# Kernel optimization log

Hardware: AMD Instinct MI355X
Metric: run time of the kernel (lower is better)

## Reference

```python
import jax, jax.numpy as jnp
import numpy as np

B, N, C = 8, 4096, 256
HEADS = 8
DH = C // HEADS
SR = 4
EPS = 1e-5


def setup_inputs() -> dict:
    key = jax.random.key(0)
    ks = jax.random.split(key, 12)
    s = 0.02
    inp = {
        "x": jax.random.normal(ks[0], (B, N, C), dtype=jnp.float32),
        "H": 64,
        "W": 64,
        # nn.Linear weights stored torch-style [out, in]
        "q_w": jax.random.normal(ks[1], (C, C), dtype=jnp.float32) * s,
        "q_b": jax.random.normal(ks[2], (C,), dtype=jnp.float32) * s,
        "kv_w": jax.random.normal(ks[3], (2 * C, C), dtype=jnp.float32) * s,
        "kv_b": jax.random.normal(ks[4], (2 * C,), dtype=jnp.float32) * s,
        # Conv2d weight torch OIHW [C, C, SR, SR]
        "sr_w": jax.random.normal(ks[5], (C, C, SR, SR), dtype=jnp.float32) * s,
        "sr_b": jax.random.normal(ks[6], (C,), dtype=jnp.float32) * s,
        "ln_g": jnp.ones((C,), dtype=jnp.float32),
        "ln_b": jnp.zeros((C,), dtype=jnp.float32),
        "proj_w": jax.random.normal(ks[7], (C, C), dtype=jnp.float32) * s,
        "proj_b": jax.random.normal(ks[8], (C,), dtype=jnp.float32) * s,
    }
    return inp


def _layernorm(x, g, b):
    mu = jnp.mean(x, axis=-1, keepdims=True)
    var = jnp.mean(jnp.square(x - mu), axis=-1, keepdims=True)
    return (x - mu) * jax.lax.rsqrt(var + EPS) * g + b


def reference(x, H, W, q_w, q_b, kv_w, kv_b, sr_w, sr_b, ln_g, ln_b, proj_w, proj_b):
    b, n, c = x.shape
    scale = 1.0 / jnp.sqrt(jnp.float32(DH))

    # q projection -> [b, heads, n, dh]
    q = (x @ q_w.T + q_b).reshape(b, n, HEADS, DH).transpose(0, 2, 1, 3)

    # spatial reduction: conv stride=SR kernel=SR on the [b,H,W,c] image
    x_img = x.reshape(b, H, W, c)  # NHWC
    kern = jnp.transpose(sr_w, (2, 3, 1, 0))  # OIHW -> HWIO
    x_sr = jax.lax.conv_general_dilated(
        x_img, kern, window_strides=(SR, SR), padding="VALID",
        dimension_numbers=("NHWC", "HWIO", "NHWC")) + sr_b
    n_kv = (H // SR) * (W // SR)
    x_sr = x_sr.reshape(b, n_kv, c)
    x_sr = _layernorm(x_sr, ln_g, ln_b)

    # kv projection -> k, v: [b, heads, n_kv, dh]
    kv = (x_sr @ kv_w.T + kv_b).reshape(b, n_kv, 2, HEADS, DH)
    kv = kv.transpose(2, 0, 3, 1, 4)
    k, v = kv[0], kv[1]

    # attention (dropout rates are 0.0 / eval mode)
    attn = jnp.einsum("bhnd,bhmd->bhnm", q, k) * scale
    attn = jax.nn.softmax(attn, axis=-1)
    out = jnp.einsum("bhnm,bhmd->bhnd", attn, v)
    out = out.transpose(0, 2, 1, 3).reshape(b, n, c)
    return out @ proj_w.T + proj_b
```

## Files before the change

### kernel.cpp

```cpp
#include <hip/hip_runtime.h>

typedef unsigned short u16;
typedef float f32x4 __attribute__((ext_vector_type(4)));
typedef __bf16 bf16x4 __attribute__((ext_vector_type(4)));
typedef __bf16 bf16x8 __attribute__((ext_vector_type(8)));

#define B_ 8
#define N_ 4096
#define C_ 256
#define NKV 256
#define CEXP 0.25506604f

__device__ inline u16 f2bf(float f) {
    union { float f; unsigned u; } v; v.f = f;
    unsigned r = v.u + 0x7FFF + ((v.u >> 16) & 1);
    return (u16)(r >> 16);
}

__device__ inline void gload16(const void* g, void* l) {
    __builtin_amdgcn_global_load_lds(
        (const __attribute__((address_space(1))) void*)g,
        (__attribute__((address_space(3))) void*)l, 16, 0, 0);
}

__global__ __launch_bounds__(256) void prep_all(
    const float* __restrict__ x, u16* __restrict__ xb,
    const float* __restrict__ qw, const float* __restrict__ kvw,
    const float* __restrict__ pw, const float* __restrict__ srw,
    u16* __restrict__ wqb, u16* __restrict__ wkv, u16* __restrict__ wp, u16* __restrict__ wsr)
{
    size_t base = ((size_t)blockIdx.x * 256 + threadIdx.x) * 4;
    float4 v = *(const float4*)(x + base);
    ushort4 o;
    o.x = f2bf(v.x); o.y = f2bf(v.y); o.z = f2bf(v.z); o.w = f2bf(v.w);
    *(ushort4*)(xb + base) = o;

    int t = blockIdx.x * 256 + threadIdx.x;
    int stride = gridDim.x * 256;
    for (int i = t; i < 65536; i += stride) { wqb[i] = f2bf(qw[i]); wp[i] = f2bf(pw[i]); }
    for (int i = t; i < 131072; i += stride) wkv[i] = f2bf(kvw[i]);
    for (int i = t; i < 1048576; i += stride) {
        int oo = i >> 12, kk = i & 4095;
        int ci = kk & 255, khkw = kk >> 8;
        wsr[i] = f2bf(srw[(size_t)(oo * 256 + ci) * 16 + khkw]);
    }
}

template<int OUTMODE, bool IM2COL>
__device__ __forceinline__ void gemm_body(
    u16* As, u16* Bs,
    const u16* __restrict__ A, const u16* __restrict__ Bt,
    const float* __restrict__ bias, void* __restrict__ outp,
    int M, int Nn, int K, int kchunk, int bm, int bn, int bz)
{
    const int tid = threadIdx.x;
    const int k0 = bz * kchunk;
    const int wid = tid >> 6, lane = tid & 63;
    const int wr = wid >> 1, wc = wid & 1;
    const int lrow = lane & 15, lkg = lane >> 4;

    f32x4 acc[4][4] = {};

    const int c1 = tid, c2 = tid + 256;
    const int r1 = c1 >> 2, cl1 = (c1 & 3) * 8;
    const int r2 = c2 >> 2, cl2 = (c2 & 3) * 8;
    const u16 *aS1, *aS2;
    if constexpr (IM2COL) {
        const int g1 = bm * 128 + r1, g2 = bm * 128 + r2;
        const int b1 = g1 >> 8, p1 = g1 & 255;
        const int b2 = g2 >> 8, p2 = g2 & 255;
        aS1 = A + ((size_t)(b1 * 4096 + (p1 >> 4) * 256 + (p1 & 15) * 4) * 256 + cl1);
        aS2 = A + ((size_t)(b2 * 4096 + (p2 >> 4) * 256 + (p2 & 15) * 4) * 256 + cl2);
    } else {
        aS1 = A + (size_t)(bm * 128 + r1) * K + k0 + cl1;
        aS2 = A + (size_t)(bm * 128 + r2) * K + k0 + cl2;
    }
    const u16* bS1 = Bt + (size_t)(bn * 128 + r1) * K + k0 + cl1;
    const u16* bS2 = Bt + (size_t)(bn * 128 + r2) * K + k0 + cl2;
    u16* aD1 = As + c1 * 8;  u16* aD2 = As + c2 * 8;
    u16* bD1 = Bs + c1 * 8;  u16* bD2 = Bs + c2 * 8;

    for (int kk = 0; kk < kchunk; kk += 32) {
        int aoff;
        if constexpr (IM2COL) {
            const int K0 = k0 + kk;
            const int khkw = K0 >> 8;
            aoff = ((khkw >> 2) * 64 + (khkw & 3)) * 256 + (K0 & 255);
        } else {
            aoff = kk;
        }
        gload16(aS1 + aoff, aD1);
        gload16(aS2 + aoff, aD2);
        gload16(bS1 + kk, bD1);
        gload16(bS2 + kk, bD2);
        __syncthreads();
        bf16x8 af[4], bff[4];
#pragma unroll
        for (int i = 0; i < 4; ++i) {
            af[i]  = *(const bf16x8*)(As + (wr * 64 + i * 16 + lrow) * 32 + lkg * 8);
            bff[i] = *(const bf16x8*)(Bs + (wc * 64 + i * 16 + lrow) * 32 + lkg * 8);
        }
#pragma unroll
        for (int i = 0; i < 4; ++i)
#pragma unroll
            for (int j = 0; j < 4; ++j)
                acc[i][j] = __builtin_amdgcn_mfma_f32_16x16x32_bf16(af[i], bff[j], acc[i][j], 0, 0, 0);
        __syncthreads();
    }

    const int row0 = bm * 128 + wr * 64;
    const int col0 = bn * 128 + wc * 64;
    if constexpr (OUTMODE == 2) {
        float* o = (float*)outp + (size_t)bz * M * Nn;
#pragma unroll
        for (int i = 0; i < 4; ++i)
#pragma unroll
            for (int j = 0; j < 4; ++j)
#pragma unroll
                for (int reg = 0; reg < 4; ++reg)
                    o[(size_t)(row0 + i * 16 + lkg * 4 + reg) * Nn + col0 + j * 16 + lrow] = acc[i][j][reg];
    } else {
#pragma unroll
        for (int j = 0; j < 4; ++j) {
            const int col = col0 + j * 16 + lrow;
            float bv = bias[col];
#pragma unroll
            for (int i = 0; i < 4; ++i)
#pragma unroll
                for (int reg = 0; reg < 4; ++reg) {
                    const size_t idx = (size_t)(row0 + i * 16 + lkg * 4 + reg) * Nn + col;
                    const float val = acc[i][j][reg] + bv;
                    if constexpr (OUTMODE == 1) ((u16*)outp)[idx] = f2bf(val);
                    else                        ((float*)outp)[idx] = val;
                }
        }
    }
}

template<int OUTMODE, bool IM2COL>
__global__ __launch_bounds__(256, 2) void gemm128(
    const u16* __restrict__ A, const u16* __restrict__ Bt,
    const float* __restrict__ bias, void* __restrict__ outp,
    int M, int Nn, int K, int kchunk)
{
    __shared__ __align__(16) u16 As[128 * 32];
    __shared__ __align__(16) u16 Bs[128 * 32];
    gemm_body<OUTMODE, IM2COL>(As, Bs, A, Bt, bias, outp, M, Nn, K, kchunk,
                               blockIdx.x, blockIdx.y, blockIdx.z);
}

__global__ __launch_bounds__(256, 2) void fused_convq(
    const u16* __restrict__ xb, const u16* __restrict__ wsr, float* __restrict__ part,
    const u16* __restrict__ wqb, const float* __restrict__ qb, u16* __restrict__ qbuf)
{
    __shared__ __align__(16) u16 As[128 * 32];
    __shared__ __align__(16) u16 Bs[128 * 32];
    const int id = blockIdx.x;
    if (id < 128) {
        const int z = id & 3, t = id >> 2;
        gemm_body<2, true>(As, Bs, xb, wsr, nullptr, part,
                           2048, 256, 4096, 1024, t >> 1, t & 1, z);
    } else {
        const int qid = id - 128;
        gemm_body<1, false>(As, Bs, xb, wqb, qb, qbuf,
                            32768, 256, 256, 256, qid >> 1, qid & 1, 0);
    }
}

__global__ __launch_bounds__(256) void ln_kernel(
    const float* __restrict__ part, const float* __restrict__ srb,
    const float* __restrict__ g, const float* __restrict__ bb, u16* __restrict__ out)
{
    const int row = blockIdx.x, c = threadIdx.x;
    const size_t idx = (size_t)row * 256 + c;
    float v = srb[c];
#pragma unroll
    for (int z = 0; z < 4; ++z) v += part[idx + (size_t)z * 524288];
    float s = v;
#pragma unroll
    for (int m = 1; m < 64; m <<= 1) s += __shfl_xor(s, m);
    __shared__ float red[4];
    if ((c & 63) == 0) red[c >> 6] = s;
    __syncthreads();
    float tot = red[0] + red[1] + red[2] + red[3];
    float mu = tot * (1.0f / 256.0f);
    float d = v - mu;
    float s2 = d * d;
#pragma unroll
    for (int m = 1; m < 64; m <<= 1) s2 += __shfl_xor(s2, m);
    __syncthreads();
    if ((c & 63) == 0) red[c >> 6] = s2;
    __syncthreads();
    float var = (red[0] + red[1] + red[2] + red[3]) * (1.0f / 256.0f);
    out[idx] = f2bf(d * rsqrtf(var + 1e-5f) * g[c] + bb[c]);
}

__global__ __launch_bounds__(256, 2) void gemm64_kv(
    const u16* __restrict__ A, const u16* __restrict__ Bt,
    const float* __restrict__ bias, u16* __restrict__ outp)
{
    __shared__ __align__(16) u16 As[64 * 32];
    __shared__ __align__(16) u16 Bs[64 * 32];
    const int tid = threadIdx.x, bm = blockIdx.x, bn = blockIdx.y;
    const int wid = tid >> 6, lane = tid & 63;
    const int wr = wid >> 1, wc = wid & 1;
    const int lrow = lane & 15, lkg = lane >> 4;

    f32x4 acc[2][2] = {};
    const int r = tid >> 2, cl = (tid & 3) * 8;
    const u16* aS = A  + (size_t)(bm * 64 + r) * 256 + cl;
    const u16* bS = Bt + (size_t)(bn * 64 + r) * 256 + cl;
    u16* aD = As + tid * 8;
    u16* bD = Bs + tid * 8;

    for (int kk = 0; kk < 256; kk += 32) {
        gload16(aS + kk, aD);
        gload16(bS + kk, bD);
        __syncthreads();
        bf16x8 af[2], bf2[2];
#pragma unroll
        for (int i = 0; i < 2; ++i) {
            af[i]  = *(const bf16x8*)(As + (wr * 32 + i * 16 + lrow) * 32 + lkg * 8);
            bf2[i] = *(const bf16x8*)(Bs + (wc * 32 + i * 16 + lrow) * 32 + lkg * 8);
        }
#pragma unroll
        for (int i = 0; i < 2; ++i)
#pragma unroll
            for (int j = 0; j < 2; ++j)
                acc[i][j] = __builtin_amdgcn_mfma_f32_16x16x32_bf16(af[i], bf2[j], acc[i][j], 0, 0, 0);
        __syncthreads();
    }

    const int row0 = bm * 64 + wr * 32;
    const int col0 = bn * 64 + wc * 32;
#pragma unroll
    for (int j = 0; j < 2; ++j) {
        const int col = col0 + j * 16 + lrow;
        const float bv = bias[col];
        const float sc = (col < 256) ? CEXP : 1.0f;
#pragma unroll
        for (int i = 0; i < 2; ++i)
#pragma unroll
            for (int reg = 0; reg < 4; ++reg)
                outp[(size_t)(row0 + i * 16 + lkg * 4 + reg) * 512 + col] =
                    f2bf((acc[i][j][reg] + bv) * sc);
    }
}

__global__ __launch_bounds__(256, 4) void attn_kernel(
    const u16* __restrict__ qbuf, const u16* __restrict__ kvbuf, u16* __restrict__ obuf)
{
    __shared__ __align__(16) u16 Ks[256 * 32];
    __shared__ __align__(16) u16 Vt[32 * 264];
    const int qt = blockIdx.x, h = blockIdx.y, b = blockIdx.z;
    const int tid = threadIdx.x;
    const int wid = tid >> 6, lane = tid & 63;
    const int lrow = lane & 15, lkg = lane >> 4;

    {
        const int loff = (lane * 16) ^ (((lane >> 3) & 7) << 4);
        const int rloc = loff >> 6, piece = (loff >> 4) & 3;
#pragma unroll
        for (int i = 0; i < 4; ++i) {
            const int c = wid * 4 + i;
            const u16* src = kvbuf + (size_t)(b * 256 + c * 16 + rloc) * 512 + h * 32 + piece * 8;
            gload16(src, Ks + c * 512);
        }
    }
    {
        const int i = tid & 127, dbase = (tid >> 7) * 16;
        const u16* vs0 = kvbuf + (size_t)(b * 256 + 2 * i) * 512 + 256 + h * 32 + dbase;
        const u16* vs1 = vs0 + 512;
        ushort4 a0 = *(const ushort4*)(vs0);
        ushort4 a1 = *(const ushort4*)(vs0 + 4);
        ushort4 a2 = *(const ushort4*)(vs0 + 8);
        ushort4 a3 = *(const ushort4*)(vs0 + 12);
        ushort4 b0 = *(const ushort4*)(vs1);
        ushort4 b1 = *(const ushort4*)(vs1 + 4);
        ushort4 b2 = *(const ushort4*)(vs1 + 8);
        ushort4 b3 = *(const ushort4*)(vs1 + 12);
        unsigned* vw = (unsigned*)(Vt + (size_t)dbase * 264 + 2 * i);
#define VPACK(d, lo, hi) vw[(d) * 132] = ((unsigned)(hi) << 16) | (lo)
        VPACK(0,  a0.x, b0.x); VPACK(1,  a0.y, b0.y); VPACK(2,  a0.z, b0.z); VPACK(3,  a0.w, b0.w);
        VPACK(4,  a1.x, b1.x); VPACK(5,  a1.y, b1.y); VPACK(6,  a1.z, b1.z); VPACK(7,  a1.w, b1.w);
        VPACK(8,  a2.x, b2.x); VPACK(9,  a2.y, b2.y); VPACK(10, a2.z, b2.z); VPACK(11, a2.w, b2.w);
        VPACK(12, a3.x, b3.x); VPACK(13, a3.y, b3.y); VPACK(14, a3.z, b3.z); VPACK(15, a3.w, b3.w);
#undef VPACK
    }

    const int qcol = h * 32 + lkg * 8;
    bf16x8 qf = *(const bf16x8*)(qbuf +
        (size_t)(b * 4096 + qt * 64 + wid * 16 + lrow) * 256 + qcol);

    bf16x8 onesf = {};
    if (lrow == 0) {
#pragma unroll
        for (int e = 0; e < 8; ++e) onesf[e] = (__bf16)1.0f;
    }

    __syncthreads();

    const int pbase = (lrow * 64 + lkg * 16) ^ (((lrow >> 1) & 7) << 4);
    f32x4 acc[16];
#pragma unroll
    for (int nf = 0; nf < 16; ++nf) acc[nf] = (f32x4){0.f, 0.f, 0.f, 0.f};
#pragma unroll
    for (int nf = 0; nf < 16; ++nf) {
        bf16x8 kfr = *(const bf16x8*)((const char*)Ks + pbase + nf * 1024);
        acc[nf] = __builtin_amdgcn_mfma_f32_16x16x32_bf16(kfr, qf, acc[nf], 0, 0, 0);
    }

    bf16x8 pa8[8];
#pragma unroll
    for (int nf2 = 0; nf2 < 8; ++nf2) {
        bf16x8 pv;
#pragma unroll
        for (int half = 0; half < 2; ++half) {
#pragma unroll
            for (int r = 0; r < 4; ++r)
                pv[half * 4 + r] = (__bf16)exp2f(acc[2 * nf2 + half][r]);
        }
        pa8[nf2] = pv;
    }

    f32x4 o0 = (f32x4){0.f, 0.f, 0.f, 0.f};
    f32x4 o1 = (f32x4){0.f, 0.f, 0.f, 0.f};
    f32x4 o2 = (f32x4){0.f, 0.f, 0.f, 0.f};
#pragma unroll
    for (int nf2 = 0; nf2 < 8; ++nf2) {
        bf16x4 lo0 = *(const bf16x4*)(Vt + lrow * 264 + nf2 * 32 + lkg * 4);
        bf16x4 hi0 = *(const bf16x4*)(Vt + lrow * 264 + nf2 * 32 + 16 + lkg * 4);
        bf16x4 lo1 = *(const bf16x4*)(Vt + (16 + lrow) * 264 + nf2 * 32 + lkg * 4);
        bf16x4 hi1 = *(const bf16x4*)(Vt + (16 + lrow) * 264 + nf2 * 32 + 16 + lkg * 4);
        bf16x8 v0 = __builtin_shufflevector(lo0, hi0, 0, 1, 2, 3, 4, 5, 6, 7);
        bf16x8 v1 = __builtin_shufflevector(lo1, hi1, 0, 1, 2, 3, 4, 5, 6, 7);
        o0 = __builtin_amdgcn_mfma_f32_16x16x32_bf16(pa8[nf2], v0, o0, 0, 0, 0);
        o1 = __builtin_amdgcn_mfma_f32_16x16x32_bf16(pa8[nf2], v1, o1, 0, 0, 0);
        o2 = __builtin_amdgcn_mfma_f32_16x16x32_bf16(pa8[nf2], onesf, o2, 0, 0, 0);
    }

    float invq[4];
#pragma unroll
    for (int r = 0; r < 4; ++r)
        invq[r] = __shfl(__builtin_amdgcn_rcpf(o2[r]), lane & 48);

    const size_t obase = (size_t)(b * 4096 + qt * 64 + wid * 16);
#pragma unroll
    for (int r = 0; r < 4; ++r) {
        u16* op = obuf + (obase + lkg * 4 + r) * 256 + h * 32 + lrow;
        op[0]  = f2bf(o0[r] * invq[r]);
        op[16] = f2bf(o1[r] * invq[r]);
    }
}

extern "C" void kernel_launch(void* const* d_in, const int* in_sizes, int n_in,
                              void* d_out, int out_size, void* d_ws, size_t ws_size,
                              hipStream_t stream)
{
    (void)in_sizes; (void)n_in; (void)out_size; (void)ws_size;
    const float* x   = (const float*)d_in[0];
    const float* qw  = (const float*)d_in[3];
    const float* qb  = (const float*)d_in[4];
    const float* kvw = (const float*)d_in[5];
    const float* kvb = (const float*)d_in[6];
    const float* srw = (const float*)d_in[7];
    const float* srb = (const float*)d_in[8];
    const float* lng = (const float*)d_in[9];
    const float* lnb = (const float*)d_in[10];
    const float* pw  = (const float*)d_in[11];
    const float* pb  = (const float*)d_in[12];

    char* ws = (char*)d_ws;
    u16*   xb      = (u16*)(ws + 0);
    u16*   att     = (u16*)(ws + 16777216);
    float* part    = (float*)(ws + 33554432);
    u16*   wsr     = (u16*)(ws + 50331648);
    u16*   wqb     = (u16*)(ws + 52428800);
    u16*   wkvb    = (u16*)(ws + 52559872);
    u16*   wpb     = (u16*)(ws + 52822016);
    u16*   xsr     = (u16*)(ws + 52953088);
    u16*   kvo     = (u16*)(ws + 54001664);
    u16*   qbuf    = (u16*)d_out;

    prep_all<<<8192, 256, 0, stream>>>(x, xb, qw, kvw, pw, srw, wqb, wkvb, wpb, wsr);
    fused_convq<<<640, 256, 0, stream>>>(xb, wsr, part, wqb, qb, qbuf);
    ln_kernel<<<2048, 256, 0, stream>>>(part, srb, lng, lnb, xsr);
    gemm64_kv<<<dim3(32, 8), 256, 0, stream>>>(xsr, wkvb, kvb, kvo);
    attn_kernel<<<dim3(64, 8, 8), 256, 0, stream>>>(qbuf, kvo, att);
    gemm128<0, false><<<dim3(256, 2, 1), 256, 0, stream>>>(att, wpb, pb, d_out, 32768, 256, 256, 256);
}
```

Before: 91.47 us.

## Fuse LayerNorm into KV projection GEMM, normalizing rows directly into LDS

Merges the separate LayerNorm kernel and the KV GEMM into one kernel. Each block reduces the split-K conv partials for its 64 rows, computes mean and variance in a single pass (E[x^2]-mu^2), and writes the bf16 normalized tile into a padded LDS buffer that serves as the full-K A operand. This removes one launch and the xsr write/read round trip. In exchange, the LayerNorm is recomputed once per N-block (8 times per row), which adds extra reads of the fp32 partials, and the single-pass variance is less numerically robust.

Result: slower. 103.9 us (+13.6%).

```diff
diff --git a/kernel.cpp b/kernel.cpp
--- a/kernel.cpp
+++ b/kernel.cpp
@@ -167,83 +167,83 @@
     }
 }
 
-__global__ __launch_bounds__(256) void ln_kernel(
+__global__ __launch_bounds__(256, 2) void ln_kv(
     const float* __restrict__ part, const float* __restrict__ srb,
-    const float* __restrict__ g, const float* __restrict__ bb, u16* __restrict__ out)
-{
-    const int row = blockIdx.x, c = threadIdx.x;
-    const size_t idx = (size_t)row * 256 + c;
-    float v = srb[c];
-#pragma unroll
-    for (int z = 0; z < 4; ++z) v += part[idx + (size_t)z * 524288];
-    float s = v;
-#pragma unroll
-    for (int m = 1; m < 64; m <<= 1) s += __shfl_xor(s, m);
-    __shared__ float red[4];
-    if ((c & 63) == 0) red[c >> 6] = s;
+    const float* __restrict__ lng, const float* __restrict__ lnb,
+    const u16* __restrict__ wkv, const float* __restrict__ kvb, u16* __restrict__ kvo)
+{
+    __shared__ __align__(16) u16 As[64 * 264];
+    __shared__ __align__(16) u16 Bs[64 * 32];
+    const int bm = blockIdx.x, bn = blockIdx.y;
+    const int tid = threadIdx.x;
+
+    {
+        const int row = tid >> 2;
+        const int cq  = (tid & 3) * 64;
+        const float* pr = part + (size_t)(bm * 64 + row) * 256 + cq;
+        float v[64];
+        float s = 0.f, s2 = 0.f;
+#pragma unroll
+        for (int j = 0; j < 16; ++j) {
+            float4 a = *(const float4*)(srb + cq + 4 * j);
+#pragma unroll
+            for (int z = 0; z < 4; ++z) {
+                float4 p = *(const float4*)(pr + (size_t)z * 524288 + 4 * j);
+                a.x += p.x; a.y += p.y; a.z += p.z; a.w += p.w;
+            }
+            v[4 * j + 0] = a.x; v[4 * j + 1] = a.y;
+            v[4 * j + 2] = a.z; v[4 * j + 3] = a.w;
+            s  += a.x + a.y + a.z + a.w;
+            s2 += a.x * a.x + a.y * a.y + a.z * a.z + a.w * a.w;
+        }
+        s  += __shfl_xor(s, 1);  s  += __shfl_xor(s, 2);
+        s2 += __shfl_xor(s2, 1); s2 += __shfl_xor(s2, 2);
+        const float mu  = s * (1.0f / 256.0f);
+        const float var = s2 * (1.0f / 256.0f) - mu * mu;
+        const float rs  = rsqrtf(fmaxf(var, 0.0f) + 1e-5f);
+        u16* dst = As + row * 264 + cq;
+#pragma unroll
+        for (int j = 0; j < 16; ++j) {
+            float4 g4 = *(const float4*)(lng + cq + 4 * j);
+            float4 b4 = *(const float4*)(lnb + cq + 4 * j);
+            ushort4 o;
+            o.x = f2bf((v[4 * j + 0] - mu) * rs * g4.x + b4.x);
+            o.y = f2bf((v[4 * j + 1] - mu) * rs * g4.y + b4.y);
+            o.z = f2bf((v[4 * j + 2] - mu) * rs * g4.z + b4.z);
+            o.w = f2bf((v[4 * j + 3] - mu) * rs * g4.w + b4.w);
+            *(ushort4*)(dst + 4 * j) = o;
+        }
+    }
     __syncthreads();
-    float tot = red[0] + red[1] + red[2] + red[3];
-    float mu = tot * (1.0f / 256.0f);
-    float d = v - mu;
-    float s2 = d * d;
-#pragma unroll
-    for (int m = 1; m < 64; m <<= 1) s2 += __shfl_xor(s2, m);
-    __syncthreads();
-    if ((c & 63) == 0) red[c >> 6] = s2;
-    __syncthreads();
-    float var = (red[0] + red[1] + red[2] + red[3]) * (1.0f / 256.0f);
-    out[idx] = f2bf(d * rsqrtf(var + 1e-5f) * g[c] + bb[c]);
-}
-
-__global__ __launch_bounds__(256, 2) void gemm64_kv(
-    const u16* __restrict__ A, const u16* __restrict__ Bt,
-    const float* __restrict__ bias, u16* __restrict__ outp)
-{
-    __shared__ __align__(16) u16 As[64 * 32];
-    __shared__ __align__(16) u16 Bs[64 * 32];
-    const int tid = threadIdx.x, bm = blockIdx.x, bn = blockIdx.y;
+
     const int wid = tid >> 6, lane = tid & 63;
-    const int wr = wid >> 1, wc = wid & 1;
     const int lrow = lane & 15, lkg = lane >> 4;
-
-    f32x4 acc[2][2] = {};
-    const int r = tid >> 2, cl = (tid & 3) * 8;
-    const u16* aS = A  + (size_t)(bm * 64 + r) * 256 + cl;
-    const u16* bS = Bt + (size_t)(bn * 64 + r) * 256 + cl;
-    u16* aD = As + tid * 8;
+    f32x4 acc[4] = {};
+
+    const u16* bS = wkv + (size_t)(bn * 64 + (tid >> 2)) * 256 + (tid & 3) * 8;
     u16* bD = Bs + tid * 8;
 
     for (int kk = 0; kk < 256; kk += 32) {
-        gload16(aS + kk, aD);
         gload16(bS + kk, bD);
         __syncthreads();
-        bf16x8 af[2], bf2[2];
-#pragma unroll
-        for (int i = 0; i < 2; ++i) {
-            af[i]  = *(const bf16x8*)(As + (wr * 32 + i * 16 + lrow) * 32 + lkg * 8);
-            bf2[i] = *(const bf16x8*)(Bs + (wc * 32 + i * 16 + lrow) * 32 + lkg * 8);
-        }
-#pragma unroll
-        for (int i = 0; i < 2; ++i)
-#pragma unroll
-            for (int j = 0; j < 2; ++j)
-                acc[i][j] = __builtin_amdgcn_mfma_f32_16x16x32_bf16(af[i], bf2[j], acc[i][j], 0, 0, 0);
+        bf16x8 af = *(const bf16x8*)(As + (wid * 16 + lrow) * 264 + kk + lkg * 8);
+#pragma unroll
+        for (int j = 0; j < 4; ++j) {
+            bf16x8 bff = *(const bf16x8*)(Bs + (j * 16 + lrow) * 32 + lkg * 8);
+            acc[j] = __builtin_amdgcn_mfma_f32_16x16x32_bf16(af, bff, acc[j], 0, 0, 0);
+        }
         __syncthreads();
     }
 
-    const int row0 = bm * 64 + wr * 32;
-    const int col0 = bn * 64 + wc * 32;
-#pragma unroll
-    for (int j = 0; j < 2; ++j) {
-        const int col = col0 + j * 16 + lrow;
-        const float bv = bias[col];
-        const float sc = (col < 256) ? CEXP : 1.0f;
-#pragma unroll
-        for (int i = 0; i < 2; ++i)
-#pragma unroll
-            for (int reg = 0; reg < 4; ++reg)
-                outp[(size_t)(row0 + i * 16 + lkg * 4 + reg) * 512 + col] =
-                    f2bf((acc[i][j][reg] + bv) * sc);
+    const int row0 = bm * 64 + wid * 16;
+    const float sc = (bn < 4) ? CEXP : 1.0f;
+#pragma unroll
+    for (int j = 0; j < 4; ++j) {
+        const int col = bn * 64 + j * 16 + lrow;
+        const float bv = kvb[col];
+#pragma unroll
+        for (int reg = 0; reg < 4; ++reg)
+            kvo[(size_t)(row0 + lkg * 4 + reg) * 512 + col] = f2bf((acc[j][reg] + bv) * sc);
     }
 }
 
@@ -378,14 +378,12 @@
     u16*   wqb     = (u16*)(ws + 52428800);
     u16*   wkvb    = (u16*)(ws + 52559872);
     u16*   wpb     = (u16*)(ws + 52822016);
-    u16*   xsr     = (u16*)(ws + 52953088);
     u16*   kvo     = (u16*)(ws + 54001664);
     u16*   qbuf    = (u16*)d_out;
 
     prep_all<<<8192, 256, 0, stream>>>(x, xb, qw, kvw, pw, srw, wqb, wkvb, wpb, wsr);
     fused_convq<<<640, 256, 0, stream>>>(xb, wsr, part, wqb, qb, qbuf);
-    ln_kernel<<<2048, 256, 0, stream>>>(part, srb, lng, lnb, xsr);
-    gemm64_kv<<<dim3(32, 8), 256, 0, stream>>>(xsr, wkvb, kvb, kvo);
+    ln_kv<<<dim3(32, 8), 256, 0, stream>>>(part, srb, lng, lnb, wkvb, kvb, kvo);
     attn_kernel<<<dim3(64, 8, 8), 256, 0, stream>>>(qbuf, kvo, att);
     gemm128<0, false><<<dim3(256, 2, 1), 256, 0, stream>>>(att, wpb, pb, d_out, 32768, 256, 256, 256);
 }
```
